# Optimization experiments

Measured on AMD Instinct MI355X. Metric: run time of the kernel, lower is better.

## Reference

```python
import jax, jax.numpy as jnp
import numpy as np

N = 50000      # nodes
E = 800000     # edges (avg degree 16)
F_IN = 32      # node_feat_dim
D = 128        # hidden_dim
L = 4          # n_layers
H = 8          # n_heads
DK = D // H    # 16
NB = 5         # n_bands
NS = 5         # n_stages
DFF = 4 * D    # ffn hidden


def setup_inputs() -> dict:
    key = jax.random.key(0)
    ks = jax.random.split(key, 24)
    s = 0.02
    inp = {}
    # forward args
    inp['x'] = jax.random.normal(ks[0], (N, F_IN), jnp.float32)
    inp['edge_index'] = jax.random.randint(ks[1], (2, E), 0, N)
    inp['edge_attr'] = jax.random.uniform(ks[2], (E,), jnp.float32)
    inp['band_ids'] = jax.random.randint(ks[3], (E,), 0, NB)
    inp['stage_ids'] = jax.random.randint(ks[4], (N,), 0, NS)
    # learned params (dropout in eval mode -> identity)
    inp['stage_emb'] = jax.random.normal(ks[5], (NS, D), jnp.float32) * s
    inp['in_w'] = jax.random.normal(ks[6], (F_IN, D), jnp.float32) * s
    inp['in_b'] = jnp.zeros((D,), jnp.float32)
    inp['Wq'] = jax.random.normal(ks[7], (L, D, D), jnp.float32) * s
    inp['Wk'] = jax.random.normal(ks[8], (L, D, D), jnp.float32) * s
    inp['Wv'] = jax.random.normal(ks[9], (L, D, D), jnp.float32) * s
    inp['Wo'] = jax.random.normal(ks[10], (L, D, D), jnp.float32) * s
    inp['Wo_b'] = jnp.zeros((L, D), jnp.float32)
    inp['band_bias'] = jax.random.normal(ks[11], (L, NB, H), jnp.float32) * s
    inp['ln1_g'] = jnp.ones((L, D), jnp.float32)
    inp['ln1_b'] = jnp.zeros((L, D), jnp.float32)
    inp['ffn_w1'] = jax.random.normal(ks[12], (L, D, DFF), jnp.float32) * s
    inp['ffn_b1'] = jnp.zeros((L, DFF), jnp.float32)
    inp['ffn_w2'] = jax.random.normal(ks[13], (L, DFF, D), jnp.float32) * s
    inp['ffn_b2'] = jnp.zeros((L, D), jnp.float32)
    inp['ln2_g'] = jnp.ones((L, D), jnp.float32)
    inp['ln2_b'] = jnp.zeros((L, D), jnp.float32)
    inp['out_w'] = jax.random.normal(ks[14], (D, D), jnp.float32) * s
    inp['out_b'] = jnp.zeros((D,), jnp.float32)
    return inp


def _layer_norm(x, g, b, eps=1e-5):
    m = x.mean(-1, keepdims=True)
    v = ((x - m) ** 2).mean(-1, keepdims=True)
    return (x - m) * jax.lax.rsqrt(v + eps) * g + b


def reference(x, edge_index, edge_attr, band_ids, stage_ids, stage_emb,
              in_w, in_b, Wq, Wk, Wv, Wo, Wo_b, band_bias,
              ln1_g, ln1_b, ffn_w1, ffn_b1, ffn_w2, ffn_b2,
              ln2_g, ln2_b, out_w, out_b):
    n = x.shape[0]
    src = edge_index[0]  # message sources (j)
    dst = edge_index[1]  # message targets (i) -> softmax / aggregation index
    scale = 1.0 / np.sqrt(DK).astype(np.float32)

    h = x @ in_w + in_b + stage_emb[stage_ids]  # (N, D)

    for l in range(L):
        Q = (h @ Wq[l]).reshape(n, H, DK)
        K = (h @ Wk[l]).reshape(n, H, DK)
        V = (h @ Wv[l]).reshape(n, H, DK)
        # edge-gather dot-product attention logits + band bias, (E, H)
        attn = jnp.einsum('ehd,ehd->eh', Q[dst], K[src]) * scale
        attn = (attn + band_bias[l][band_ids]) * edge_attr[:, None]
        # segment softmax over edges sharing the same destination node
        mx = jax.ops.segment_max(attn, dst, num_segments=n)  # (N, H)
        ex = jnp.exp(attn - mx[dst])
        sm = jax.ops.segment_sum(ex, dst, num_segments=n)
        a = ex / (sm[dst] + 1e-16)  # (E, H)
        # weighted scatter-add of V_j into destination nodes
        agg = jax.ops.segment_sum(a[:, :, None] * V[src], dst, num_segments=n)
        o = agg.reshape(n, D) @ Wo[l] + Wo_b[l]
        h = _layer_norm(o + h, ln1_g[l], ln1_b[l])  # residual (in_dim == out_dim)
        ff = jax.nn.gelu(h @ ffn_w1[l] + ffn_b1[l], approximate=False) @ ffn_w2[l] + ffn_b2[l]
        h = _layer_norm(h + ff, ln2_g[l], ln2_b[l])

    return h @ out_w + out_b
```

## Files before the change

kernel.cpp:

```cpp
#include <hip/hip_runtime.h>
#include <math.h>

constexpr int N_   = 50000;
constexpr int E_   = 800000;
constexpr int FIN_ = 32;
constexpr int D_   = 128;
constexpr int H_   = 8;
constexpr int NB_  = 5;
constexpr int L_   = 4;
constexpr int DFF_ = 512;

typedef __attribute__((ext_vector_type(8))) short short8;
typedef __attribute__((ext_vector_type(4))) short short4v;
typedef __attribute__((ext_vector_type(4))) float f32x4;
typedef __attribute__((ext_vector_type(2))) float f32x2;

__device__ __forceinline__ short f2bf(float f){
  unsigned u = __float_as_uint(f);
  unsigned r = (u + 0x7FFFu + ((u >> 16) & 1u)) >> 16;
  return (short)r;
}
__device__ __forceinline__ float bf2f(short v){
  return __uint_as_float(((unsigned)(unsigned short)v) << 16);
}
__device__ __forceinline__ float bflo(unsigned u){ return __uint_as_float(u << 16); }
__device__ __forceinline__ float bfhi(unsigned u){ return __uint_as_float(u & 0xffff0000u); }

__device__ __forceinline__ unsigned char f2fp8(float x){
  int p = __builtin_amdgcn_cvt_pk_fp8_f32(x, x, 0, false);
  return (unsigned char)(p & 0xFF);
}

__device__ __forceinline__ float gelu_f(float x){
  float xs = x * 0.70710678118654752f;
  float ax = fabsf(xs);
  float t  = __builtin_amdgcn_rcpf(1.0f + 0.3275911f*ax);
  float y  = t*(0.254829592f + t*(-0.284496736f + t*(1.421413741f +
             t*(-1.453152027f + t*1.061405429f))));
  float e  = exp2f(-ax*ax*1.4426950408889634f);
  float er = 1.0f - y*e;
  er = __uint_as_float((__float_as_uint(er) & 0x7fffffffu) |
                       (__float_as_uint(xs) & 0x80000000u));
  return 0.5f*x*(1.0f + er);
}

__device__ __forceinline__ size_t pfidx(int n, int k, int K){
  return ((size_t)(n >> 4)*(2*K) + (size_t)(k >> 3)*16 + (n & 15))*8 + (k & 7);
}

__global__ __launch_bounds__(256)
void conv_weights(const float* __restrict__ Wq, const float* __restrict__ Wk,
                  const float* __restrict__ Wv, const float* __restrict__ Wo,
                  const float* __restrict__ w1, const float* __restrict__ w2,
                  const float* __restrict__ ow,
                  short* __restrict__ wqkvt, short* __restrict__ wot,
                  short* __restrict__ w1t, short* __restrict__ w2t,
                  short* __restrict__ owt){
  int idx = blockIdx.x * blockDim.x + threadIdx.x;
  if (idx < 3*L_*16384){
    int m = idx / (L_*16384);
    int r = idx % (L_*16384);
    int l = r / 16384, e = r % 16384;
    int k = e >> 7, n = e & 127;
    const float* src = (m == 0) ? Wq : ((m == 1) ? Wk : Wv);
    wqkvt[(size_t)(l*3 + m)*16384 + pfidx(n, k, 128)] = f2bf(src[(size_t)l*16384 + e]);
    return;
  }
  idx -= 3*L_*16384;
  if (idx < L_*16384){
    int l = idx / 16384, e = idx % 16384, k = e >> 7, n = e & 127;
    wot[(size_t)l*16384 + pfidx(n, k, 128)] = f2bf(Wo[idx]);
    return;
  }
  idx -= L_*16384;
  if (idx < L_*D_*DFF_){
    int l = idx / 65536, e = idx % 65536;
    int k = e >> 9, n = e & 511;
    w1t[(size_t)l*65536 + pfidx(n, k, 128)] = f2bf(w1[idx]);
    return;
  }
  idx -= L_*D_*DFF_;
  if (idx < L_*DFF_*D_){
    int l = idx / 65536, e = idx % 65536;
    int k = e >> 7, n = e & 127;
    w2t[(size_t)l*65536 + pfidx(n, k, 512)] = f2bf(w2[idx]);
    return;
  }
  idx -= L_*DFF_*D_;
  if (idx < 16384){
    int k = idx >> 7, n = idx & 127;
    owt[pfidx(n, k, 128)] = f2bf(ow[idx]);
  }
}

__global__ __launch_bounds__(256)
void input_proj(const float* __restrict__ x, const float* __restrict__ in_w,
                const float* __restrict__ in_b, const float* __restrict__ se,
                const int* __restrict__ sid, short* __restrict__ hb){
  int sub = threadIdx.x >> 7, d = threadIdx.x & 127;
  int i = blockIdx.x*2 + sub;
  __shared__ float xs[2][FIN_];
  if (d < FIN_) xs[sub][d] = x[(size_t)i*FIN_ + d];
  __syncthreads();
  float acc = in_b[d] + se[(size_t)sid[i]*D_ + d];
  #pragma unroll 8
  for (int k=0;k<FIN_;k++) acc += xs[sub][k]*in_w[k*D_+d];
  hb[(size_t)i*D_+d] = f2bf(acc);
}

__global__ void k_deg(const int* __restrict__ dst, const int* __restrict__ src,
                      const int* __restrict__ band,
                      int* __restrict__ deg, int* __restrict__ pk){
  int e = blockIdx.x*blockDim.x + threadIdx.x;
  if (e < E_){
    atomicAdd(&deg[dst[e]], 1);
    pk[e] = src[e] | (band[e] << 16);
  }
}

__global__ __launch_bounds__(1024)
void k_scan1(const int* __restrict__ deg, int* __restrict__ rowptr,
             int* __restrict__ bsum){
  __shared__ int sm[1024];
  int b = blockIdx.x, tid = threadIdx.x;
  int i = b*1024 + tid;
  int v = (i < N_) ? deg[i] : 0;
  sm[tid] = v; __syncthreads();
  for (int off=1; off<1024; off<<=1){
    int t = (tid>=off) ? sm[tid-off] : 0;
    __syncthreads();
    sm[tid] += t;
    __syncthreads();
  }
  if (i < N_) rowptr[i+1] = sm[tid];
  if (tid == 1023) bsum[b] = sm[1023];
}

__global__ void k_scan2(int* __restrict__ bsum, int nb){
  int tid = threadIdx.x;
  int v = (tid < nb) ? bsum[tid] : 0;
  for (int off=1; off<64; off<<=1){
    int t = __shfl_up(v, off, 64);
    if (tid >= off) v += t;
  }
  if (tid < nb) bsum[tid] = v;
}

__global__ void k_scan3(int* __restrict__ rowptr, const int* __restrict__ bsum){
  int i = blockIdx.x*blockDim.x + threadIdx.x;
  if (i == 0) rowptr[0] = 0;
  if (i < N_){
    int b = i >> 10;
    if (b > 0) rowptr[i+1] += bsum[b-1];
  }
}

__global__ void k_scatter(const int* __restrict__ dst, const int* __restrict__ rowptr,
                          int* __restrict__ fill, int* __restrict__ eord){
  int e = blockIdx.x*blockDim.x + threadIdx.x;
  if (e < E_){
    int d = dst[e];
    int pos = rowptr[d] + atomicAdd(&fill[d], 1);
    eord[pos] = e;
  }
}

__global__ void k_sortseg(const int* __restrict__ rowptr, int* __restrict__ eord){
  int i = blockIdx.x*blockDim.x + threadIdx.x;
  if (i >= N_) return;
  int b = rowptr[i], t = rowptr[i+1];
  for (int p = b+1; p < t; p++){
    int v = eord[p];
    int q = p-1;
    while (q >= b && eord[q] > v){ eord[q+1] = eord[q]; q--; }
    eord[q+1] = v;
  }
}

__global__ void k_emeta(const int* __restrict__ eord, const int* __restrict__ pk,
                        const float* __restrict__ eattr, int2* __restrict__ em){
  int p = blockIdx.x*blockDim.x + threadIdx.x;
  if (p < E_){
    int e = eord[p];
    em[p] = make_int2(pk[e], __float_as_int(eattr[e]));
  }
}

template<int EPI>
__global__ __launch_bounds__(512, 2)
void gemm128_direct(const short* __restrict__ A, const short* __restrict__ Wt,
                    const float* __restrict__ bias,
                    float* Cf, short* Yb, unsigned char* KV8, int M, long wstride){
  const int tid = threadIdx.x;
  const int by  = blockIdx.y;
  Wt += (size_t)by * wstride;
  const short8* W8 = (const short8*)Wt;
  const int m0 = blockIdx.x * 128;
  const int lane = tid & 63, w = tid >> 6;
  const int wr = w >> 2, wc = w & 3;
  const int lrow = lane & 15, lgrp = lane >> 4;
  f32x4 acc[4][2];
  #pragma unroll
  for (int r=0;r<4;r++){ acc[r][0] = {0.f,0.f,0.f,0.f}; acc[r][1] = {0.f,0.f,0.f,0.f}; }
  int rowA[4];
  #pragma unroll
  for (int r=0;r<4;r++){
    int rr = m0 + wr*64 + r*16 + lrow;
    rowA[r] = (rr < M) ? rr : (M-1);
  }
  #pragma unroll
  for (int kk = 0; kk < 4; kk++){
    const int koff = kk*32 + lgrp*8;
    short8 af[4], bfr[2];
    #pragma unroll
    for (int r = 0; r < 4; r++)
      af[r] = *(const short8*)(A + (size_t)rowA[r]*128 + koff);
    #pragma unroll
    for (int c = 0; c < 2; c++)
      bfr[c] = W8[(size_t)(wc*2 + c)*256 + kk*64 + lane];
    #pragma unroll
    for (int r = 0; r < 4; r++)
      #pragma unroll
      for (int c = 0; c < 2; c++)
        acc[r][c] = __builtin_amdgcn_mfma_f32_16x16x32_bf16(af[r], bfr[c], acc[r][c], 0, 0, 0);
  }
  #pragma unroll
  for (int r = 0; r < 4; r++){
    #pragma unroll
    for (int c = 0; c < 2; c++){
      int col = wc*32 + c*16 + lrow;
      float bv = (EPI == 3) ? bias[col] : 0.f;
      #pragma unroll
      for (int v = 0; v < 4; v++){
        int row = m0 + wr*64 + r*16 + lgrp*4 + v;
        if (row < M){
          float o = acc[r][c][v] + bv;
          if (EPI == 3) Cf[(size_t)row*128 + col] = o;
          else if (by == 0) Yb[(size_t)row*128 + col] = f2bf(o);
          else KV8[(size_t)row*256 + (by-1)*128 + col] = f2fp8(o);
        }
      }
    }
  }
}

__global__ __launch_bounds__(256, 4)
void wo_ffn_fused(const short* __restrict__ aggb, const short* __restrict__ wot,
                  const float* __restrict__ wo_b, short* __restrict__ hb,
                  const short* __restrict__ w1t, const float* __restrict__ b1,
                  const short* __restrict__ w2t, const float* __restrict__ b2,
                  const float* __restrict__ g1, const float* __restrict__ bl1,
                  const float* __restrict__ g2, const float* __restrict__ bl2,
                  const short* __restrict__ qkvw,
                  short* __restrict__ qb, unsigned char* __restrict__ kv8,
                  int M){
  __shared__ char ytile[8192];
  __shared__ char hidb[8192];
  __shared__ float rsum[4][32];
  __shared__ float rsq[4][32];
  const int tid = threadIdx.x;
  const int m0 = blockIdx.x * 32;
  const int lane = tid & 63, w = tid >> 6;
  const int lrow = lane & 15, lgrp = lane >> 4;
  int rowA[2];
  #pragma unroll
  for (int r=0;r<2;r++){
    int rr = m0 + r*16 + lrow;
    rowA[r] = (rr < M) ? rr : (M-1);
  }

  {
    const short8* W8 = (const short8*)wot;
    f32x4 acc[2][2];
    #pragma unroll
    for (int r=0;r<2;r++){ acc[r][0] = {0.f,0.f,0.f,0.f}; acc[r][1] = {0.f,0.f,0.f,0.f}; }
    #pragma unroll
    for (int kk = 0; kk < 4; kk++){
      const int koff = kk*32 + lgrp*8;
      short8 af[2], bfr[2];
      #pragma unroll
      for (int r = 0; r < 2; r++)
        af[r] = *(const short8*)(aggb + (size_t)rowA[r]*128 + koff);
      #pragma unroll
      for (int c = 0; c < 2; c++)
        bfr[c] = W8[(size_t)(w*2 + c)*256 + kk*64 + lane];
      #pragma unroll
      for (int r = 0; r < 2; r++)
        #pragma unroll
        for (int c = 0; c < 2; c++)
          acc[r][c] = __builtin_amdgcn_mfma_f32_16x16x32_bf16(af[r], bfr[c], acc[r][c], 0, 0, 0);
    }
    float ps[2][4], pq[2][4];
    #pragma unroll
    for (int r=0;r<2;r++)
      #pragma unroll
      for (int v=0;v<4;v++){ ps[r][v]=0.f; pq[r][v]=0.f; }
    #pragma unroll
    for (int r = 0; r < 2; r++){
      #pragma unroll
      for (int c = 0; c < 2; c++){
        int col = w*32 + c*16 + lrow;
        float bv = wo_b[col];
        #pragma unroll
        for (int v = 0; v < 4; v++){
          int grow = m0 + r*16 + lgrp*4 + v;
          int gr = (grow < M) ? grow : (M-1);
          float oo = acc[r][c][v] + bv + bf2f(hb[(size_t)gr*128 + col]);
          ps[r][v] += oo;
          pq[r][v] += oo*oo;
          int row = r*16 + lgrp*4 + v;
          int off = row*256 + col*2;
          *(short*)(ytile + (off ^ ((row & 7) << 4))) = f2bf(oo);
        }
      }
    }
    #pragma unroll
    for (int r = 0; r < 2; r++)
      #pragma unroll
      for (int v = 0; v < 4; v++){
        #pragma unroll
        for (int off = 1; off < 16; off <<= 1){
          ps[r][v] += __shfl_xor(ps[r][v], off, 16);
          pq[r][v] += __shfl_xor(pq[r][v], off, 16);
        }
      }
    if (lrow == 0){
      #pragma unroll
      for (int r = 0; r < 2; r++)
        #pragma unroll
        for (int v = 0; v < 4; v++){
          int row = r*16 + lgrp*4 + v;
          rsum[w][row] = ps[r][v];
          rsq[w][row]  = pq[r][v];
        }
    }
    __syncthreads();
    #pragma unroll
    for (int r = 0; r < 2; r++){
      float gv[2], bv2[2];
      #pragma unroll
      for (int c = 0; c < 2; c++){
        int col = w*32 + c*16 + lrow;
        gv[c] = g1[col]; bv2[c] = bl1[col];
      }
      #pragma unroll
      for (int v = 0; v < 4; v++){
        int row = r*16 + lgrp*4 + v;
        float s = (rsum[0][row]+rsum[1][row]) + (rsum[2][row]+rsum[3][row]);
        float q = (rsq[0][row]+rsq[1][row]) + (rsq[2][row]+rsq[3][row]);
        float mean = s * (1.f/128.f);
        float var  = q * (1.f/128.f) - mean*mean;
        float rstd = rsqrtf(var + 1e-5f);
        #pragma unroll
        for (int c = 0; c < 2; c++){
          int col = w*32 + c*16 + lrow;
          int off = row*256 + col*2;
          float oo = bf2f(*(const short*)(ytile + (off ^ ((row & 7) << 4))));
          float y = (oo - mean)*rstd*gv[c] + bv2[c];
          *(short*)(ytile + (off ^ ((row & 7) << 4))) = f2bf(y);
        }
      }
    }
  }
  __syncthreads();

  const short8* W18 = (const short8*)w1t;
  const short8* W28 = (const short8*)w2t;
  f32x4 acc2[2][2];
  #pragma unroll
  for (int r=0;r<2;r++){ acc2[r][0] = {0.f,0.f,0.f,0.f}; acc2[r][1] = {0.f,0.f,0.f,0.f}; }
  #pragma unroll
  for (int chunk = 0; chunk < 4; chunk++){
    f32x4 acc1[2][2];
    #pragma unroll
    for (int r=0;r<2;r++){ acc1[r][0] = {0.f,0.f,0.f,0.f}; acc1[r][1] = {0.f,0.f,0.f,0.f}; }
    #pragma unroll
    for (int kk = 0; kk < 4; kk++){
      const int kbyt = kk*64 + lgrp*16;
      short8 af[2], bfr[2];
      #pragma unroll
      for (int r = 0; r < 2; r++){
        int row = r*16 + lrow;
        af[r] = *(const short8*)(ytile + ((row*256 + kbyt) ^ ((row & 7) << 4)));
      }
      #pragma unroll
      for (int c = 0; c < 2; c++){
        int nb = chunk*8 + w*2 + c;
        bfr[c] = W18[(size_t)nb*256 + kk*64 + lane];
      }
      #pragma unroll
      for (int r = 0; r < 2; r++)
        #pragma unroll
        for (int c = 0; c < 2; c++)
          acc1[r][c] = __builtin_amdgcn_mfma_f32_16x16x32_bf16(af[r], bfr[c], acc1[r][c], 0, 0, 0);
    }
    __syncthreads();
    #pragma unroll
    for (int r = 0; r < 2; r++){
      #pragma unroll
      for (int c = 0; c < 2; c++){
        int lc = w*32 + c*16 + lrow;
        float bv = b1[chunk*128 + lc];
        #pragma unroll
        for (int v = 0; v < 4; v++){
          int row = r*16 + lgrp*4 + v;
          float g = gelu_f(acc1[r][c][v] + bv);
          int off = row*256 + lc*2;
          *(short*)(hidb + (off ^ ((row & 7) << 4))) = f2bf(g);
        }
      }
    }
    __syncthreads();
    #pragma unroll
    for (int kk2 = 0; kk2 < 4; kk2++){
      short8 ah[2], bh[2];
      #pragma unroll
      for (int r = 0; r < 2; r++){
        int row = r*16 + lrow;
        ah[r] = *(const short8*)(hidb + ((row*256 + kk2*64 + lgrp*16) ^ ((row & 7) << 4)));
      }
      #pragma unroll
      for (int c = 0; c < 2; c++){
        int nb = w*2 + c;
        bh[c] = W28[(size_t)nb*1024 + chunk*256 + kk2*64 + lane];
      }
      #pragma unroll
      for (int r = 0; r < 2; r++)
        #pragma unroll
        for (int c = 0; c < 2; c++)
          acc2[r][c] = __builtin_amdgcn_mfma_f32_16x16x32_bf16(ah[r], bh[c], acc2[r][c], 0, 0, 0);
    }
  }

  {
    float ps[2][4], pq[2][4];
    #pragma unroll
    for (int r=0;r<2;r++)
      #pragma unroll
      for (int v=0;v<4;v++){ ps[r][v]=0.f; pq[r][v]=0.f; }
    #pragma unroll
    for (int r = 0; r < 2; r++){
      #pragma unroll
      for (int c = 0; c < 2; c++){
        int col = w*32 + c*16 + lrow;
        float bv = b2[col];
        #pragma unroll
        for (int v = 0; v < 4; v++){
          int row = r*16 + lgrp*4 + v;
          int off = row*256 + col*2;
          float res = bf2f(*(const short*)(ytile + (off ^ ((row & 7) << 4))));
          float oo = acc2[r][c][v] + bv + res;
          ps[r][v] += oo;
          pq[r][v] += oo*oo;
          *(short*)(ytile + (off ^ ((row & 7) << 4))) = f2bf(oo);
        }
      }
    }
    #pragma unroll
    for (int r = 0; r < 2; r++)
      #pragma unroll
      for (int v = 0; v < 4; v++){
        #pragma unroll
        for (int off = 1; off < 16; off <<= 1){
          ps[r][v] += __shfl_xor(ps[r][v], off, 16);
          pq[r][v] += __shfl_xor(pq[r][v], off, 16);
        }
      }
    __syncthreads();
    if (lrow == 0){
      #pragma unroll
      for (int r = 0; r < 2; r++)
        #pragma unroll
        for (int v = 0; v < 4; v++){
          int row = r*16 + lgrp*4 + v;
          rsum[w][row] = ps[r][v];
          rsq[w][row]  = pq[r][v];
        }
    }
    __syncthreads();
    #pragma unroll
    for (int r = 0; r < 2; r++){
      float gv[2], bv2[2];
      #pragma unroll
      for (int c = 0; c < 2; c++){
        int col = w*32 + c*16 + lrow;
        gv[c] = g2[col]; bv2[c] = bl2[col];
      }
      #pragma unroll
      for (int v = 0; v < 4; v++){
        int row = r*16 + lgrp*4 + v;
        int grow = m0 + row;
        float s = (rsum[0][row]+rsum[1][row]) + (rsum[2][row]+rsum[3][row]);
        float q = (rsq[0][row]+rsq[1][row]) + (rsq[2][row]+rsq[3][row]);
        float mean = s * (1.f/128.f);
        float var  = q * (1.f/128.f) - mean*mean;
        float rstd = rsqrtf(var + 1e-5f);
        #pragma unroll
        for (int c = 0; c < 2; c++){
          int col = w*32 + c*16 + lrow;
          int off = row*256 + col*2;
          float oo = bf2f(*(const short*)(ytile + (off ^ ((row & 7) << 4))));
          float y = (oo - mean)*rstd*gv[c] + bv2[c];
          if (grow < M) hb[(size_t)grow*128 + col] = f2bf(y);
          *(short*)(ytile + (off ^ ((row & 7) << 4))) = f2bf(y);
        }
      }
    }
  }

  if (qkvw != nullptr){
    __syncthreads();
    #pragma unroll
    for (int m = 0; m < 3; m++){
      const short8* Wm = (const short8*)(qkvw + (size_t)m*16384);
      f32x4 accq[2][2];
      #pragma unroll
      for (int r=0;r<2;r++){ accq[r][0] = {0.f,0.f,0.f,0.f}; accq[r][1] = {0.f,0.f,0.f,0.f}; }
      #pragma unroll
      for (int kk = 0; kk < 4; kk++){
        const int kbyt = kk*64 + lgrp*16;
        short8 af[2], bfr[2];
        #pragma unroll
        for (int r = 0; r < 2; r++){
          int row = r*16 + lrow;
          af[r] = *(const short8*)(ytile + ((row*256 + kbyt) ^ ((row & 7) << 4)));
        }
        #pragma unroll
        for (int c = 0; c < 2; c++)
          bfr[c] = Wm[(size_t)(w*2 + c)*256 + kk*64 + lane];
        #pragma unroll
        for (int r = 0; r < 2; r++)
          #pragma unroll
          for (int c = 0; c < 2; c++)
            accq[r][c] = __builtin_amdgcn_mfma_f32_16x16x32_bf16(af[r], bfr[c], accq[r][c], 0, 0, 0);
      }
      #pragma unroll
      for (int r = 0; r < 2; r++){
        #pragma unroll
        for (int c = 0; c < 2; c++){
          int col = w*32 + c*16 + lrow;
          #pragma unroll
          for (int v = 0; v < 4; v++){
            int grow = m0 + r*16 + lgrp*4 + v;
            if (grow < M){
              float o = accq[r][c][v];
              if (m == 0) qb[(size_t)grow*128 + col] = f2bf(o);
              else        kv8[(size_t)grow*256 + (m-1)*128 + col] = f2fp8(o);
            }
          }
        }
      }
    }
  }
}

__global__ __launch_bounds__(256, 8)
void attn_fused(const short* __restrict__ Qb, const unsigned char* __restrict__ KV8,
                const int2* __restrict__ em,
                const int* __restrict__ rowptr,
                const float* __restrict__ bb_l, short* __restrict__ aggb){
  const int lane = threadIdx.x & 63;
  const int i = (blockIdx.x << 2) + (threadIdx.x >> 6);
  if (i >= N_) return;
  const int hh = lane >> 3;
  const unsigned qw = ((const unsigned*)Qb)[(size_t)i*64 + lane];
  const float q0 = bflo(qw), q1 = bfhi(qw);
  const int p0 = __builtin_amdgcn_readfirstlane(rowptr[i]);
  const int p1 = __builtin_amdgcn_readfirstlane(rowptr[i+1]);
  constexpr float L2E = 1.442695040888963f;
  float2 outv = {0.f, 0.f};
  if (p0 < p1){
    float s[4]; float2 acc[4];
    #pragma unroll
    for (int c=0;c<4;c++){ s[c]=0.f; acc[c].x=0.f; acc[c].y=0.f; }
    int sj[4], sjN[4];
    float bb[4], ea[4], bbN[4], eaN[4];
    int kw[4], vw[4], kwN[4], vwN[4];

    auto ldmeta = [&](int gb, int* SJ, float* BB, float* EA){
      #pragma unroll
      for (int c = 0; c < 4; c++){
        int idx = gb + c; idx = (idx < p1) ? idx : (p1 - 1);
        int2 m = em[idx];
        unsigned u = (unsigned)__builtin_amdgcn_readfirstlane(m.x);
        SJ[c] = (int)(u & 0xFFFFu);
        BB[c] = bb_l[(u >> 16)*H_ + hh];
        EA[c] = __uint_as_float((unsigned)__builtin_amdgcn_readfirstlane(m.y));
      }
    };

    ldmeta(p0, sj, bb, ea);
    #pragma unroll
    for (int c = 0; c < 4; c++){
      kw[c] = *(const unsigned short*)(KV8 + (size_t)sj[c]*256 + lane*2);
      vw[c] = *(const unsigned short*)(KV8 + (size_t)sj[c]*256 + 128 + lane*2);
    }
    ldmeta(p0 + 4, sjN, bbN, eaN);

    for (int base = p0; base < p1; base += 4){
      #pragma unroll
      for (int c = 0; c < 4; c++){
        kwN[c] = *(const unsigned short*)(KV8 + (size_t)sjN[c]*256 + lane*2);
        vwN[c] = *(const unsigned short*)(KV8 + (size_t)sjN[c]*256 + 128 + lane*2);
      }
      int sj2[4]; float bb2[4], ea2[4];
      ldmeta(base + 8, sj2, bb2, ea2);
      #pragma unroll
      for (int c = 0; c < 4; c++){
        f32x2 kf = __builtin_amdgcn_cvt_pk_f32_fp8(kw[c], false);
        float dot = q0*kf[0] + q1*kf[1];
        dot += __shfl_xor(dot, 1, 8);
        dot += __shfl_xor(dot, 2, 8);
        dot += __shfl_xor(dot, 4, 8);
        float logit = (dot*0.25f + bb[c]) * ea[c];
        logit = fminf(logit, 60.f);
        if (base + c >= p1) logit = -1.0e30f;
        float wgt = exp2f(logit * L2E);
        f32x2 vf = __builtin_amdgcn_cvt_pk_f32_fp8(vw[c], false);
        s[c]     += wgt;
        acc[c].x += wgt*vf[0];
        acc[c].y += wgt*vf[1];
      }
      #pragma unroll
      for (int c = 0; c < 4; c++){
        kw[c]=kwN[c]; vw[c]=vwN[c];
        sj[c]=sjN[c]; bb[c]=bbN[c]; ea[c]=eaN[c];
        sjN[c]=sj2[c]; bbN[c]=bb2[c]; eaN[c]=ea2[c];
      }
    }
    float S = (s[0]+s[1]) + (s[2]+s[3]);
    float Ax = (acc[0].x+acc[1].x) + (acc[2].x+acc[3].x);
    float Ay = (acc[0].y+acc[1].y) + (acc[2].y+acc[3].y);
    float inv = 1.0f / (S + 1e-16f);
    outv.x = Ax * inv;
    outv.y = Ay * inv;
  }
  unsigned lo = (unsigned)(unsigned short)f2bf(outv.x);
  unsigned hi = (unsigned)(unsigned short)f2bf(outv.y);
  ((unsigned*)aggb)[(size_t)i*64 + lane] = lo | (hi << 16);
}

extern "C" void kernel_launch(void* const* d_in, const int* in_sizes, int n_in,
                              void* d_out, int out_size, void* d_ws, size_t ws_size,
                              hipStream_t stream) {
  const float* x         = (const float*)d_in[0];
  const int*   edge_index= (const int*)  d_in[1];
  const float* edge_attr = (const float*)d_in[2];
  const int*   band_ids  = (const int*)  d_in[3];
  const int*   stage_ids = (const int*)  d_in[4];
  const float* stage_emb = (const float*)d_in[5];
  const float* in_w      = (const float*)d_in[6];
  const float* in_b      = (const float*)d_in[7];
  const float* Wq        = (const float*)d_in[8];
  const float* Wk        = (const float*)d_in[9];
  const float* Wv        = (const float*)d_in[10];
  const float* Wo        = (const float*)d_in[11];
  const float* Wo_b      = (const float*)d_in[12];
  const float* band_bias = (const float*)d_in[13];
  const float* ln1_g     = (const float*)d_in[14];
  const float* ln1_b     = (const float*)d_in[15];
  const float* ffn_w1    = (const float*)d_in[16];
  const float* ffn_b1    = (const float*)d_in[17];
  const float* ffn_w2    = (const float*)d_in[18];
  const float* ffn_b2    = (const float*)d_in[19];
  const float* ln2_g     = (const float*)d_in[20];
  const float* ln2_b     = (const float*)d_in[21];
  const float* out_w     = (const float*)d_in[22];
  const float* out_b     = (const float*)d_in[23];
  float* out = (float*)d_out;

  const size_t ND = (size_t)N_*D_;
  float* ws  = (float*)d_ws;
  short* hb   = (short*)ws;
  short* aggb = (short*)(ws + ND);
  short* qb   = (short*)(ws + 2*ND);
  unsigned char* kv8 = (unsigned char*)(ws + 2*ND + ND/2);
  short* wbuf = (short*)(ws + 3*ND + ND/2);
  short* wqkvt = wbuf;
  short* wot   = wbuf + 196608;
  short* w1t   = wbuf + 262144;
  short* w2t   = wbuf + 524288;
  short* owt   = wbuf + 786432;
  int*  ibase = (int*)(ws + 3*ND + ND/2 + 401408);
  int*  deg   = ibase;
  int*  fill  = ibase + N_;
  int*  rowptr= ibase + 2*N_;
  int*  eord  = ibase + 3*N_ + 1;
  int*  bsum  = ibase + 3*N_ + 1 + E_;
  int*  pk    = ibase + 3*N_ + 1 + E_ + 64;
  int2* em    = (int2*)(ibase + 3*N_ + 1 + 2*E_ + 64);

  const int* srcA = edge_index;
  const int* dstA = edge_index + E_;

  hipMemsetAsync(deg, 0, 2ull*N_*sizeof(int), stream);

  conv_weights<<<3136, 256, 0, stream>>>(Wq, Wk, Wv, Wo, ffn_w1, ffn_w2, out_w,
                                         wqkvt, wot, w1t, w2t, owt);
  input_proj<<<N_/2, 256, 0, stream>>>(x, in_w, in_b, stage_emb, stage_ids, hb);

  k_deg   <<<(E_+255)/256, 256, 0, stream>>>(dstA, srcA, band_ids, deg, pk);
  k_scan1 <<<49, 1024, 0, stream>>>(deg, rowptr, bsum);
  k_scan2 <<<1, 64, 0, stream>>>(bsum, 49);
  k_scan3 <<<(N_+255)/256, 256, 0, stream>>>(rowptr, bsum);
  k_scatter<<<(E_+255)/256, 256, 0, stream>>>(dstA, rowptr, fill, eord);
  k_sortseg<<<(N_+255)/256, 256, 0, stream>>>(rowptr, eord);
  k_emeta <<<(E_+255)/256, 256, 0, stream>>>(eord, pk, edge_attr, em);

  const int GB  = (N_ + 127) / 128;
  const int GB3 = (N_ + 31) / 32;
  const int AB  = (N_ + 3) / 4;

  gemm128_direct<4><<<dim3(GB,3), 512, 0, stream>>>(
      hb, wqkvt, nullptr, nullptr, qb, kv8, N_, 16384L);

  for (int l = 0; l < L_; l++){
    attn_fused<<<AB, 256, 0, stream>>>(qb, kv8, em, rowptr,
                                       band_bias + l*NB_*H_, aggb);

    const short* qkvw_next = (l < L_-1) ? (wqkvt + (size_t)(l+1)*3*16384) : nullptr;
    wo_ffn_fused<<<GB3, 256, 0, stream>>>(
        aggb, wot + (size_t)l*16384, Wo_b + l*D_, hb,
        w1t + (size_t)l*65536, ffn_b1 + l*DFF_,
        w2t + (size_t)l*65536, ffn_b2 + l*D_,
        ln1_g + l*D_, ln1_b + l*D_, ln2_g + l*D_, ln2_b + l*D_,
        qkvw_next, qb, kv8, N_);
  }

  gemm128_direct<3><<<GB, 512, 0, stream>>>(
      hb, owt, out_b, out, nullptr, nullptr, N_, 0L);
}
```

Measured before the change: 660.8 us.

## Double wo_ffn_fused row tile to 64 with 512-thread blocks

The fused Wo+LN+FFN+LN+QKV kernel now processes 64 rows per block using 8 waves arranged as 2 row-groups by 4 column-groups, instead of 32 rows with 4 waves. Each weight fragment loaded from global memory is meant to be shared across twice as many rows per block, halving the grid size and cutting redundant weight traffic. Shared memory per block doubles to about 34 KB and launch bounds change to (512, 8), which constrains register allocation and may lower occupancy or cause spills.

```diff
diff --git a/kernel.cpp b/kernel.cpp
--- a/kernel.cpp
+++ b/kernel.cpp
@@ -244,7 +244,7 @@
   }
 }
 
-__global__ __launch_bounds__(256, 4)
+__global__ __launch_bounds__(512, 8)
 void wo_ffn_fused(const short* __restrict__ aggb, const short* __restrict__ wot,
                   const float* __restrict__ wo_b, short* __restrict__ hb,
                   const short* __restrict__ w1t, const float* __restrict__ b1,
@@ -254,18 +254,20 @@
                   const short* __restrict__ qkvw,
                   short* __restrict__ qb, unsigned char* __restrict__ kv8,
                   int M){
-  __shared__ char ytile[8192];
-  __shared__ char hidb[8192];
-  __shared__ float rsum[4][32];
-  __shared__ float rsq[4][32];
+  __shared__ char ytile[16384];
+  __shared__ char hidb[16384];
+  __shared__ float rsum[4][64];
+  __shared__ float rsq[4][64];
   const int tid = threadIdx.x;
-  const int m0 = blockIdx.x * 32;
+  const int m0 = blockIdx.x * 64;
   const int lane = tid & 63, w = tid >> 6;
+  const int cw = w & 3, rw = w >> 2;
   const int lrow = lane & 15, lgrp = lane >> 4;
+  const int rbase = rw*32;
   int rowA[2];
   #pragma unroll
   for (int r=0;r<2;r++){
-    int rr = m0 + r*16 + lrow;
+    int rr = m0 + rbase + r*16 + lrow;
     rowA[r] = (rr < M) ? rr : (M-1);
   }
 
@@ -283,7 +285,7 @@
         af[r] = *(const short8*)(aggb + (size_t)rowA[r]*128 + koff);
       #pragma unroll
       for (int c = 0; c < 2; c++)
-        bfr[c] = W8[(size_t)(w*2 + c)*256 + kk*64 + lane];
+        bfr[c] = W8[(size_t)(cw*2 + c)*256 + kk*64 + lane];
       #pragma unroll
       for (int r = 0; r < 2; r++)
         #pragma unroll
@@ -299,16 +301,16 @@
     for (int r = 0; r < 2; r++){
       #pragma unroll
       for (int c = 0; c < 2; c++){
-        int col = w*32 + c*16 + lrow;
+        int col = cw*32 + c*16 + lrow;
         float bv = wo_b[col];
         #pragma unroll
         for (int v = 0; v < 4; v++){
-          int grow = m0 + r*16 + lgrp*4 + v;
+          int grow = m0 + rbase + r*16 + lgrp*4 + v;
           int gr = (grow < M) ? grow : (M-1);
           float oo = acc[r][c][v] + bv + bf2f(hb[(size_t)gr*128 + col]);
           ps[r][v] += oo;
           pq[r][v] += oo*oo;
-          int row = r*16 + lgrp*4 + v;
+          int row = rbase + r*16 + lgrp*4 + v;
           int off = row*256 + col*2;
           *(short*)(ytile + (off ^ ((row & 7) << 4))) = f2bf(oo);
         }
@@ -329,9 +331,9 @@
       for (int r = 0; r < 2; r++)
         #pragma unroll
         for (int v = 0; v < 4; v++){
-          int row = r*16 + lgrp*4 + v;
-          rsum[w][row] = ps[r][v];
-          rsq[w][row]  = pq[r][v];
+          int row = rbase + r*16 + lgrp*4 + v;
+          rsum[cw][row] = ps[r][v];
+          rsq[cw][row]  = pq[r][v];
         }
     }
     __syncthreads();
@@ -340,12 +342,12 @@
       float gv[2], bv2[2];
       #pragma unroll
       for (int c = 0; c < 2; c++){
-        int col = w*32 + c*16 + lrow;
+        int col = cw*32 + c*16 + lrow;
         gv[c] = g1[col]; bv2[c] = bl1[col];
       }
       #pragma unroll
       for (int v = 0; v < 4; v++){
-        int row = r*16 + lgrp*4 + v;
+        int row = rbase + r*16 + lgrp*4 + v;
         float s = (rsum[0][row]+rsum[1][row]) + (rsum[2][row]+rsum[3][row]);
         float q = (rsq[0][row]+rsq[1][row]) + (rsq[2][row]+rsq[3][row]);
         float mean = s * (1.f/128.f);
@@ -353,7 +355,7 @@
         float rstd = rsqrtf(var + 1e-5f);
         #pragma unroll
         for (int c = 0; c < 2; c++){
-          int col = w*32 + c*16 + lrow;
+          int col = cw*32 + c*16 + lrow;
           int off = row*256 + col*2;
           float oo = bf2f(*(const short*)(ytile + (off ^ ((row & 7) << 4))));
           float y = (oo - mean)*rstd*gv[c] + bv2[c];
@@ -380,12 +382,12 @@
       short8 af[2], bfr[2];
       #pragma unroll
       for (int r = 0; r < 2; r++){
-        int row = r*16 + lrow;
+        int row = rbase + r*16 + lrow;
         af[r] = *(const short8*)(ytile + ((row*256 + kbyt) ^ ((row & 7) << 4)));
       }
       #pragma unroll
       for (int c = 0; c < 2; c++){
-        int nb = chunk*8 + w*2 + c;
+        int nb = chunk*8 + cw*2 + c;
         bfr[c] = W18[(size_t)nb*256 + kk*64 + lane];
       }
       #pragma unroll
@@ -399,11 +401,11 @@
     for (int r = 0; r < 2; r++){
       #pragma unroll
       for (int c = 0; c < 2; c++){
-        int lc = w*32 + c*16 + lrow;
+        int lc = cw*32 + c*16 + lrow;
         float bv = b1[chunk*128 + lc];
         #pragma unroll
         for (int v = 0; v < 4; v++){
-          int row = r*16 + lgrp*4 + v;
+          int row = rbase + r*16 + lgrp*4 + v;
           float g = gelu_f(acc1[r][c][v] + bv);
           int off = row*256 + lc*2;
           *(short*)(hidb + (off ^ ((row & 7) << 4))) = f2bf(g);
@@ -416,12 +418,12 @@
       short8 ah[2], bh[2];
       #pragma unroll
       for (int r = 0; r < 2; r++){
-        int row = r*16 + lrow;
+        int row = rbase + r*16 + lrow;
         ah[r] = *(const short8*)(hidb + ((row*256 + kk2*64 + lgrp*16) ^ ((row & 7) << 4)));
       }
       #pragma unroll
       for (int c = 0; c < 2; c++){
-        int nb = w*2 + c;
+        int nb = cw*2 + c;
         bh[c] = W28[(size_t)nb*1024 + chunk*256 + kk2*64 + lane];
       }
       #pragma unroll
@@ -442,11 +444,11 @@
     for (int r = 0; r < 2; r++){
       #pragma unroll
       for (int c = 0; c < 2; c++){
-        int col = w*32 + c*16 + lrow;
+        int col = cw*32 + c*16 + lrow;
         float bv = b2[col];
         #pragma unroll
         for (int v = 0; v < 4; v++){
-          int row = r*16 + lgrp*4 + v;
+          int row = rbase + r*16 + lgrp*4 + v;
           int off = row*256 + col*2;
           float res = bf2f(*(const short*)(ytile + (off ^ ((row & 7) << 4))));
           float oo = acc2[r][c][v] + bv + res;
@@ -472,9 +474,9 @@
       for (int r = 0; r < 2; r++)
         #pragma unroll
         for (int v = 0; v < 4; v++){
-          int row = r*16 + lgrp*4 + v;
-          rsum[w][row] = ps[r][v];
-          rsq[w][row]  = pq[r][v];
+          int row = rbase + r*16 + lgrp*4 + v;
+          rsum[cw][row] = ps[r][v];
+          rsq[cw][row]  = pq[r][v];
         }
     }
     __syncthreads();
@@ -483,12 +485,12 @@
       float gv[2], bv2[2];
       #pragma unroll
       for (int c = 0; c < 2; c++){
-        int col = w*32 + c*16 + lrow;
+        int col = cw*32 + c*16 + lrow;
         gv[c] = g2[col]; bv2[c] = bl2[col];
       }
       #pragma unroll
       for (int v = 0; v < 4; v++){
-        int row = r*16 + lgrp*4 + v;
+        int row = rbase + r*16 + lgrp*4 + v;
         int grow = m0 + row;
         float s = (rsum[0][row]+rsum[1][row]) + (rsum[2][row]+rsum[3][row]);
         float q = (rsq[0][row]+rsq[1][row]) + (rsq[2][row]+rsq[3][row]);
@@ -497,7 +499,7 @@
         float rstd = rsqrtf(var + 1e-5f);
         #pragma unroll
         for (int c = 0; c < 2; c++){
-          int col = w*32 + c*16 + lrow;
+          int col = cw*32 + c*16 + lrow;
           int off = row*256 + col*2;
           float oo = bf2f(*(const short*)(ytile + (off ^ ((row & 7) << 4))));
           float y = (oo - mean)*rstd*gv[c] + bv2[c];
@@ -522,12 +524,12 @@
         short8 af[2], bfr[2];
         #pragma unroll
         for (int r = 0; r < 2; r++){
-          int row = r*16 + lrow;
+          int row = rbase + r*16 + lrow;
           af[r] = *(const short8*)(ytile + ((row*256 + kbyt) ^ ((row & 7) << 4)));
         }
         #pragma unroll
         for (int c = 0; c < 2; c++)
-          bfr[c] = Wm[(size_t)(w*2 + c)*256 + kk*64 + lane];
+          bfr[c] = Wm[(size_t)(cw*2 + c)*256 + kk*64 + lane];
         #pragma unroll
         for (int r = 0; r < 2; r++)
           #pragma unroll
@@ -538,10 +540,10 @@
       for (int r = 0; r < 2; r++){
         #pragma unroll
         for (int c = 0; c < 2; c++){
-          int col = w*32 + c*16 + lrow;
+          int col = cw*32 + c*16 + lrow;
           #pragma unroll
           for (int v = 0; v < 4; v++){
-            int grow = m0 + r*16 + lgrp*4 + v;
+            int grow = m0 + rbase + r*16 + lgrp*4 + v;
             if (grow < M){
               float o = accq[r][c][v];
               if (m == 0) qb[(size_t)grow*128 + col] = f2bf(o);
@@ -708,7 +710,7 @@
   k_emeta <<<(E_+255)/256, 256, 0, stream>>>(eord, pk, edge_attr, em);
 
   const int GB  = (N_ + 127) / 128;
-  const int GB3 = (N_ + 31) / 32;
+  const int GB3 = (N_ + 63) / 64;
   const int AB  = (N_ + 3) / 4;
 
   gemm128_direct<4><<<dim3(GB,3), 512, 0, stream>>>(
@@ -719,7 +721,7 @@
                                        band_bias + l*NB_*H_, aggb);
 
     const short* qkvw_next = (l < L_-1) ? (wqkvt + (size_t)(l+1)*3*16384) : nullptr;
-    wo_ffn_fused<<<GB3, 256, 0, stream>>>(
+    wo_ffn_fused<<<GB3, 512, 0, stream>>>(
         aggb, wot + (size_t)l*16384, Wo_b + l*D_, hb,
         w1t + (size_t)l*65536, ffn_b1 + l*DFF_,
         w2t + (size_t)l*65536, ffn_b2 + l*D_,
```

Measured after the change: 916.2 us. +38.6%, slower.
